# Performance work log

Hardware: AMD Instinct MI355X
Metric: run time of the kernel (lower is better)

Reference implementation:

```python
import jax, jax.numpy as jnp
import numpy as np

D_K = 64  # per-head dim, used as softmax scale (matches __init__ d_k)

def setup_inputs() -> dict:
    key = jax.random.key(0)
    kq, kk, kv, km = jax.random.split(key, 4)
    B, H, S, D = 2, 16, 2048, D_K
    q = jax.random.normal(kq, (B, H, S, D), dtype=jnp.float32)
    k = jax.random.normal(kk, (B, H, S, D), dtype=jnp.float32)
    v = jax.random.normal(kv, (B, H, S, D), dtype=jnp.float32)
    mask = jax.random.randint(km, (B, 1, S, S), 0, 2).astype(jnp.bool_)
    return {"q": q, "k": k, "v": v, "mask": mask}

def reference(q, k, v, mask):
    # attn = (q / sqrt(d_k)) @ k^T  -> [B,H,S,S]
    scale = 1.0 / jnp.sqrt(jnp.float32(D_K))
    attn = jnp.einsum("bhqd,bhkd->bhqk", q * scale, k)
    # faithful to torch masked_fill(mask, -1e-09) -- note tiny value, not -1e9
    attn = jnp.where(mask, jnp.float32(-1e-9), attn)
    weights = jax.nn.softmax(attn, axis=-1)  # dropout p=0.0 -> identity
    output = jnp.einsum("bhqk,bhkd->bhqd", weights, v)
    return (output, weights)
```

## Files before the change

### kernel.cpp

```cpp
#include <hip/hip_runtime.h>
#include <hip/hip_bf16.h>


namespace {

constexpr int kS = 2048;
constexpr int kD = 64;
constexpr int kBH = 32;
constexpr int kTQW = 16;
constexpr int kNW = 4;
constexpr int kTQB = kTQW * kNW;
constexpr int kChunk = 64;
constexpr int kNC = kS / kChunk;
constexpr int kNB = kBH * (kS / kTQB);
constexpr size_t kWOff = (size_t)kBH * kS * kD;

typedef __attribute__((ext_vector_type(8))) short bf16x8;
typedef __attribute__((ext_vector_type(4))) float f32x4;
typedef __attribute__((ext_vector_type(2))) unsigned u32x2;

__device__ inline short f2bf(float f) {
  union { float f; unsigned u; } x; x.f = f;
  return (short)((x.u + 0x7fffu + ((x.u >> 16) & 1u)) >> 16);
}

__device__ inline unsigned pk2bf(float a, float b) {
  return (unsigned)(unsigned short)f2bf(a) | ((unsigned)(unsigned short)f2bf(b) << 16);
}

__device__ inline bf16x8 cvt8(float4 a, float4 b, float scale) {
  bf16x8 f;
  f[0] = f2bf(a.x * scale); f[1] = f2bf(a.y * scale);
  f[2] = f2bf(a.z * scale); f[3] = f2bf(a.w * scale);
  f[4] = f2bf(b.x * scale); f[5] = f2bf(b.y * scale);
  f[6] = f2bf(b.z * scale); f[7] = f2bf(b.w * scale);
  return f;
}

__device__ inline void block_sync_lds() {
  asm volatile("s_waitcnt lgkmcnt(0)" ::: "memory");
  __builtin_amdgcn_s_barrier();
  asm volatile("" ::: "memory");
}

__global__ __launch_bounds__(256, 4) void attn_fused(
    const float* __restrict__ qg, const float* __restrict__ kg,
    const float* __restrict__ vg, const unsigned int* __restrict__ mg,
    float* __restrict__ outg) {
  __shared__ __align__(16) short SH[16384];
  short (*Kt0)[72] = (short(*)[72])SH;
  short (*Kt1)[72] = (short(*)[72])(SH + 4608);
  short (*Wts)[72] = (short(*)[72])(SH + 9216);
  unsigned char (*Msk0)[80] = (unsigned char(*)[80])(SH + 13824);
  unsigned char (*Msk1)[80] = (unsigned char(*)[80])(SH + 9216);

  const int tid  = threadIdx.x;
  const int wv   = tid >> 6;
  const int lane = tid & 63;
  const int l15  = lane & 15;
  const int quad = lane >> 4;

  const int bid  = blockIdx.x;
  const int work = ((bid & 7) << 7) | (bid >> 3);
  const int qt   = work & 31;
  const int bh   = work >> 5;
  const int b    = bh >> 4;
  const int q0b  = qt * kTQB;

  int allW32 = 1, allI32 = 1, allBF = 1;
#pragma unroll
  for (int i = 0; i < 64; ++i) {
    const unsigned u = mg[i];
    const unsigned lo = u & 0xFFFFu, hi = u >> 16;
    allW32 &= (int)(u == 0u || u == 0x3F800000u);
    allI32 &= (int)(u == 0u || u == 1u);
    allBF  &= (int)((lo == 0u || lo == 0x3F80u) && (hi == 0u || hi == 0x3F80u));
  }
  int msz;
  if (allI32)      msz = 4;
  else if (allW32) msz = 4;
  else if (allBF)  msz = 2;
  else             msz = 1;
  const unsigned char* mB = (const unsigned char*)mg + (size_t)b * kS * kS * msz;

  const float* qbase = qg + (size_t)bh * kS * kD;
  const float* kbase = kg + (size_t)bh * kS * kD;
  const float* vbase = vg + (size_t)bh * kS * kD;
  float* obase = outg + (size_t)bh * kS * kD;
  float* wbase = outg + kWOff + (size_t)bh * kS * kS;

  const int qrow = q0b + wv * kTQW + l15;
  const int mrow = wv * kTQW + l15;

  bf16x8 aq[2];
#pragma unroll
  for (int dh = 0; dh < 2; ++dh) {
    const float* p = qbase + (size_t)qrow * kD + dh * 32 + quad * 8;
    aq[dh] = cvt8(*(const float4*)p, *(const float4*)(p + 4), 0.125f);
  }

  const int si = tid >> 2;
  const int sj = (tid & 3) << 4;
  const int vd = (tid & 7) << 3;
  const int vk = (tid >> 3) << 1;
  float4 rk[4], rv[4];
  uint4 rmq;

  auto k_issue = [&](int c) {
    const float* p = kbase + (size_t)(c * kChunk + si) * kD + sj;
    rk[0] = *(const float4*)p;       rk[1] = *(const float4*)(p + 4);
    rk[2] = *(const float4*)(p + 8); rk[3] = *(const float4*)(p + 12);
  };
  auto k_write = [&](short (*Kdst)[72]) {
    *(bf16x8*)&Kdst[si][sj]     = cvt8(rk[0], rk[1], 1.0f);
    *(bf16x8*)&Kdst[si][sj + 8] = cvt8(rk[2], rk[3], 1.0f);
  };

  auto v_issue = [&](int c) {
    const float* p = vbase + (size_t)(c * kChunk + vk) * kD + vd;
    rv[0] = *(const float4*)p;        rv[1] = *(const float4*)(p + 4);
    rv[2] = *(const float4*)(p + kD); rv[3] = *(const float4*)(p + kD + 4);
  };
  auto v_write = [&]() {
    const float* lo = (const float*)&rv[0];
    const float* hi = (const float*)&rv[2];
#pragma unroll
    for (int d = 0; d < 8; ++d) {
      const int dd = vd + d;
      const int ps = (vk >> 1) ^ (((dd >> 3) & 7) << 2);
      const unsigned u = pk2bf(lo[d], hi[d]);
      *(unsigned*)&Kt1[dd][2 * ps] = u;
    }
  };

  auto m_issue = [&](int c) {
    if (msz == 1)
      rmq = *(const uint4*)(mB + (size_t)(q0b + si) * kS + (size_t)(c * kChunk + sj));
  };
  auto m_write = [&](unsigned char (*Mdst)[80], int c) {
    if (msz == 1) {
      *(uint4*)&Mdst[si][sj] = rmq;
    } else if (msz == 4) {
      const size_t eoff = (size_t)(q0b + si) * kS + (size_t)(c * kChunk + sj);
      const unsigned int* p = (const unsigned int*)mB + eoff;
      unsigned int* dst = (unsigned int*)&Mdst[si][sj];
#pragma unroll
      for (int g = 0; g < 4; ++g) {
        uint4 e = *(const uint4*)(p + 4 * g);
        dst[g] = (e.x ? 1u : 0u) | ((e.y ? 1u : 0u) << 8) |
                 ((e.z ? 1u : 0u) << 16) | ((e.w ? 1u : 0u) << 24);
      }
    } else {
      const size_t eoff = (size_t)(q0b + si) * kS + (size_t)(c * kChunk + sj);
      const unsigned int* p = (const unsigned int*)((const unsigned short*)mB + eoff);
      unsigned int* dst = (unsigned int*)&Mdst[si][sj];
#pragma unroll
      for (int g = 0; g < 4; ++g) {
        const unsigned int a = p[2 * g], cc = p[2 * g + 1];
        dst[g] = ((a & 0xFFFFu) ? 1u : 0u) | (((a >> 16) ? 1u : 0u) << 8) |
                 (((cc & 0xFFFFu) ? 1u : 0u) << 16) | (((cc >> 16) ? 1u : 0u) << 24);
      }
    }
  };

  float lsum = 0.f;
  k_issue(0); m_issue(0);
  k_write(Kt0); m_write(Msk0, 0);
  k_issue(1); m_issue(1);
  block_sync_lds();
  for (int c = 0; c < kNC; ++c) {
    short (*K)[72] = (c & 1) ? Kt1 : Kt0;
    const unsigned char (*M)[80] =
        (c & 1) ? (const unsigned char (*)[80])Msk1 : (const unsigned char (*)[80])Msk0;
    if (c + 1 < kNC) { k_write((c & 1) ? Kt0 : Kt1); m_write((c & 1) ? Msk0 : Msk1, c + 1); }
    if (c + 2 < kNC) { k_issue(c + 2); m_issue(c + 2); }
#pragma unroll
    for (int t = 0; t < 4; ++t) {
      bf16x8 f0 = *(const bf16x8*)&K[t * 16 + l15][quad * 8];
      bf16x8 f1 = *(const bf16x8*)&K[t * 16 + l15][32 + quad * 8];
      f32x4 acc = {0.f, 0.f, 0.f, 0.f};
      acc = __builtin_amdgcn_mfma_f32_16x16x32_bf16(f0, aq[0], acc, 0, 0, 0);
      acc = __builtin_amdgcn_mfma_f32_16x16x32_bf16(f1, aq[1], acc, 0, 0, 0);
      const unsigned mu = *(const unsigned*)&M[mrow][t * 16 + quad * 4];
#pragma unroll
      for (int r = 0; r < 4; ++r) {
        const float e = __expf(acc[r]);
        lsum += ((mu >> (8 * r)) & 0xFFu) ? 1.0f : e;
      }
    }
    block_sync_lds();
  }

  lsum += __shfl_xor(lsum, 16);
  lsum += __shfl_xor(lsum, 32);
  const float inv = 1.0f / lsum;

  f32x4 acco[4];
#pragma unroll
  for (int d = 0; d < 4; ++d) acco[d] = (f32x4){0.f, 0.f, 0.f, 0.f};

  k_issue(0); v_issue(0); m_issue(0);
  k_write(Kt0); v_write(); m_write(Msk0, 0);
  k_issue(1); v_issue(1); m_issue(1);
  block_sync_lds();
  float* const wrow = wbase + (size_t)qrow * kS;
  const int swz = (l15 & 7) << 3;
  for (int c = 0; c < kNC; ++c) {
#pragma unroll
    for (int t = 0; t < 4; ++t) {
      bf16x8 f0 = *(const bf16x8*)&Kt0[t * 16 + l15][quad * 8];
      bf16x8 f1 = *(const bf16x8*)&Kt0[t * 16 + l15][32 + quad * 8];
      f32x4 acc = {0.f, 0.f, 0.f, 0.f};
      acc = __builtin_amdgcn_mfma_f32_16x16x32_bf16(f0, aq[0], acc, 0, 0, 0);
      acc = __builtin_amdgcn_mfma_f32_16x16x32_bf16(f1, aq[1], acc, 0, 0, 0);
      const unsigned mu = *(const unsigned*)&Msk0[mrow][t * 16 + quad * 4];
      const float w0 = ((mu       & 0xFFu) ? 1.0f : __expf(acc[0])) * inv;
      const float w1 = ((mu >> 8  & 0xFFu) ? 1.0f : __expf(acc[1])) * inv;
      const float w2 = ((mu >> 16 & 0xFFu) ? 1.0f : __expf(acc[2])) * inv;
      const float w3 = ((mu >> 24        ) ? 1.0f : __expf(acc[3])) * inv;
      u32x2 uu = {pk2bf(w0, w1), pk2bf(w2, w3)};
      *(u32x2*)&Wts[wv * kTQW + l15][(t * 16 + quad * 4) ^ swz] = uu;
      f32x4 wq = {w0, w1, w2, w3};
      __builtin_nontemporal_store(wq, (f32x4*)(wrow + c * kChunk + t * 16 + quad * 4));
    }
    __builtin_amdgcn_s_setprio(1);
#pragma unroll
    for (int ks = 0; ks < 2; ++ks) {
      bf16x8 aw = *(const bf16x8*)&Wts[wv * kTQW + l15][(ks * 32 + quad * 8) ^ swz];
#pragma unroll
      for (int dt = 0; dt < 4; ++dt) {
        const int dd = dt * 16 + l15;
        const int psb = (ks * 16 + quad * 4) ^ (((dd >> 3) & 7) << 2);
        bf16x8 bv = *(const bf16x8*)&Kt1[dd][2 * psb];
        acco[dt] = __builtin_amdgcn_mfma_f32_16x16x32_bf16(bv, aw, acco[dt], 0, 0, 0);
      }
    }
    __builtin_amdgcn_s_setprio(0);
    block_sync_lds();
    if (c + 1 < kNC) { k_write(Kt0); v_write(); m_write(Msk0, c + 1); }
    if (c + 2 < kNC) { k_issue(c + 2); v_issue(c + 2); m_issue(c + 2); }
    block_sync_lds();
  }

#pragma unroll
  for (int dt = 0; dt < 4; ++dt) {
    f32x4 o = acco[dt];
    __builtin_nontemporal_store(o, (f32x4*)(obase + (size_t)qrow * kD + dt * 16 + quad * 4));
  }
}

}

extern "C" void kernel_launch(void* const* d_in, const int* in_sizes, int n_in,
                              void* d_out, int out_size, void* d_ws, size_t ws_size,
                              hipStream_t stream) {
  const float* q = (const float*)d_in[0];
  const float* k = (const float*)d_in[1];
  const float* v = (const float*)d_in[2];
  const unsigned int* mask = (const unsigned int*)d_in[3];
  float* out = (float*)d_out;
  attn_fused<<<dim3(kNB), dim3(256), 0, stream>>>(q, k, v, mask, out);
}
```

Measured before the change: 830.9 us.

## Double-buffer K/V in pass two, load mask into registers, feed PV MFMA from registers

The second pass now double-buffers both K and V in LDS with a single barrier per chunk, where it previously used one buffer and two barriers. The mask is read directly from global memory into per-lane registers instead of being staged through LDS. Probabilities are passed straight from the QK accumulator layout into 16x16x16 bf16 MFMAs for the PV product, which removes the weight round-trip through LDS. In exchange it issues twice as many smaller MFMAs, makes uncoalesced per-lane mask loads, and replaces the nontemporal weight stores with regular ones.

```diff
diff --git a/kernel.cpp b/kernel.cpp
--- a/kernel.cpp
+++ b/kernel.cpp
@@ -16,8 +16,8 @@
 constexpr size_t kWOff = (size_t)kBH * kS * kD;
 
 typedef __attribute__((ext_vector_type(8))) short bf16x8;
+typedef __attribute__((ext_vector_type(4))) short bf16x4;
 typedef __attribute__((ext_vector_type(4))) float f32x4;
-typedef __attribute__((ext_vector_type(2))) unsigned u32x2;
 
 __device__ inline short f2bf(float f) {
   union { float f; unsigned u; } x; x.f = f;
@@ -37,6 +37,22 @@
   return f;
 }
 
+__device__ inline f32x4 mfma32(bf16x8 a, bf16x8 b, f32x4 c) {
+  return __builtin_amdgcn_mfma_f32_16x16x32_bf16(a, b, c, 0, 0, 0);
+}
+
+__device__ inline f32x4 mfma16(bf16x4 a, bf16x4 b, f32x4 c) {
+#if __has_builtin(__builtin_amdgcn_mfma_f32_16x16x16bf16_1k)
+  return __builtin_amdgcn_mfma_f32_16x16x16bf16_1k(a, b, c, 0, 0, 0);
+#elif __has_builtin(__builtin_amdgcn_mfma_f32_16x16x16_bf16)
+  return __builtin_amdgcn_mfma_f32_16x16x16_bf16(a, b, c, 0, 0, 0);
+#else
+  f32x4 d = c;
+  asm volatile("v_mfma_f32_16x16x16_bf16 %0, %1, %2, %0" : "+v"(d) : "v"(a), "v"(b));
+  return d;
+#endif
+}
+
 __device__ inline void block_sync_lds() {
   asm volatile("s_waitcnt lgkmcnt(0)" ::: "memory");
   __builtin_amdgcn_s_barrier();
@@ -47,12 +63,11 @@
     const float* __restrict__ qg, const float* __restrict__ kg,
     const float* __restrict__ vg, const unsigned int* __restrict__ mg,
     float* __restrict__ outg) {
-  __shared__ __align__(16) short SH[16384];
-  short (*Kt0)[72] = (short(*)[72])SH;
-  short (*Kt1)[72] = (short(*)[72])(SH + 4608);
-  short (*Wts)[72] = (short(*)[72])(SH + 9216);
-  unsigned char (*Msk0)[80] = (unsigned char(*)[80])(SH + 13824);
-  unsigned char (*Msk1)[80] = (unsigned char(*)[80])(SH + 9216);
+  __shared__ __align__(16) short SH[18432];
+  short (*K0)[72] = (short(*)[72])(SH);
+  short (*K1)[72] = (short(*)[72])(SH + 4608);
+  short (*V0)[72] = (short(*)[72])(SH + 9216);
+  short (*V1)[72] = (short(*)[72])(SH + 13824);
 
   const int tid  = threadIdx.x;
   const int wv   = tid >> 6;
@@ -90,7 +105,6 @@
   float* wbase = outg + kWOff + (size_t)bh * kS * kS;
 
   const int qrow = q0b + wv * kTQW + l15;
-  const int mrow = wv * kTQW + l15;
 
   bf16x8 aq[2];
 #pragma unroll
@@ -104,7 +118,6 @@
   const int vd = (tid & 7) << 3;
   const int vk = (tid >> 3) << 1;
   float4 rk[4], rv[4];
-  uint4 rmq;
 
   auto k_issue = [&](int c) {
     const float* p = kbase + (size_t)(c * kChunk + si) * kD + sj;
@@ -121,71 +134,66 @@
     rv[0] = *(const float4*)p;        rv[1] = *(const float4*)(p + 4);
     rv[2] = *(const float4*)(p + kD); rv[3] = *(const float4*)(p + kD + 4);
   };
-  auto v_write = [&]() {
+  auto v_write = [&](short (*Vdst)[72]) {
     const float* lo = (const float*)&rv[0];
     const float* hi = (const float*)&rv[2];
 #pragma unroll
     for (int d = 0; d < 8; ++d) {
       const int dd = vd + d;
       const int ps = (vk >> 1) ^ (((dd >> 3) & 7) << 2);
-      const unsigned u = pk2bf(lo[d], hi[d]);
-      *(unsigned*)&Kt1[dd][2 * ps] = u;
-    }
-  };
-
+      *(unsigned*)&Vdst[dd][2 * ps] = pk2bf(lo[d], hi[d]);
+    }
+  };
+
+  uint4 mr[4];
+  unsigned mu[4];
   auto m_issue = [&](int c) {
-    if (msz == 1)
-      rmq = *(const uint4*)(mB + (size_t)(q0b + si) * kS + (size_t)(c * kChunk + sj));
-  };
-  auto m_write = [&](unsigned char (*Mdst)[80], int c) {
-    if (msz == 1) {
-      *(uint4*)&Mdst[si][sj] = rmq;
-    } else if (msz == 4) {
-      const size_t eoff = (size_t)(q0b + si) * kS + (size_t)(c * kChunk + sj);
-      const unsigned int* p = (const unsigned int*)mB + eoff;
-      unsigned int* dst = (unsigned int*)&Mdst[si][sj];
-#pragma unroll
-      for (int g = 0; g < 4; ++g) {
-        uint4 e = *(const uint4*)(p + 4 * g);
-        dst[g] = (e.x ? 1u : 0u) | ((e.y ? 1u : 0u) << 8) |
-                 ((e.z ? 1u : 0u) << 16) | ((e.w ? 1u : 0u) << 24);
-      }
-    } else {
-      const size_t eoff = (size_t)(q0b + si) * kS + (size_t)(c * kChunk + sj);
-      const unsigned int* p = (const unsigned int*)((const unsigned short*)mB + eoff);
-      unsigned int* dst = (unsigned int*)&Mdst[si][sj];
-#pragma unroll
-      for (int g = 0; g < 4; ++g) {
-        const unsigned int a = p[2 * g], cc = p[2 * g + 1];
-        dst[g] = ((a & 0xFFFFu) ? 1u : 0u) | (((a >> 16) ? 1u : 0u) << 8) |
-                 (((cc & 0xFFFFu) ? 1u : 0u) << 16) | (((cc >> 16) ? 1u : 0u) << 24);
+    const int col0 = c * kChunk + quad * 4;
+#pragma unroll
+    for (int t = 0; t < 4; ++t) {
+      const size_t e = (size_t)qrow * kS + col0 + t * 16;
+      if (msz == 1)      mr[t].x = *(const unsigned*)(mB + e);
+      else if (msz == 4) mr[t]   = *(const uint4*)((const unsigned*)mB + e);
+      else {
+        const unsigned* p = (const unsigned*)((const unsigned short*)mB + e);
+        mr[t].x = p[0]; mr[t].y = p[1];
+      }
+    }
+  };
+  auto m_conv = [&]() {
+#pragma unroll
+    for (int t = 0; t < 4; ++t) {
+      if (msz == 1)      mu[t] = mr[t].x;
+      else if (msz == 4) mu[t] = (mr[t].x ? 1u : 0u) | ((mr[t].y ? 1u : 0u) << 8) |
+                                 ((mr[t].z ? 1u : 0u) << 16) | ((mr[t].w ? 1u : 0u) << 24);
+      else {
+        const unsigned a = mr[t].x, bb = mr[t].y;
+        mu[t] = ((a & 0xFFFFu) ? 1u : 0u) | (((a >> 16) ? 1u : 0u) << 8) |
+                (((bb & 0xFFFFu) ? 1u : 0u) << 16) | (((bb >> 16) ? 1u : 0u) << 24);
       }
     }
   };
 
   float lsum = 0.f;
-  k_issue(0); m_issue(0);
-  k_write(Kt0); m_write(Msk0, 0);
-  k_issue(1); m_issue(1);
+  k_issue(0); k_write(K0); k_issue(1);
   block_sync_lds();
   for (int c = 0; c < kNC; ++c) {
-    short (*K)[72] = (c & 1) ? Kt1 : Kt0;
-    const unsigned char (*M)[80] =
-        (c & 1) ? (const unsigned char (*)[80])Msk1 : (const unsigned char (*)[80])Msk0;
-    if (c + 1 < kNC) { k_write((c & 1) ? Kt0 : Kt1); m_write((c & 1) ? Msk0 : Msk1, c + 1); }
-    if (c + 2 < kNC) { k_issue(c + 2); m_issue(c + 2); }
+    m_issue(c);
+    if (c + 1 < kNC) k_write((c & 1) ? K0 : K1);
+    if (c + 2 < kNC) k_issue(c + 2);
+    m_conv();
+    short (*K)[72] = (c & 1) ? K1 : K0;
 #pragma unroll
     for (int t = 0; t < 4; ++t) {
       bf16x8 f0 = *(const bf16x8*)&K[t * 16 + l15][quad * 8];
       bf16x8 f1 = *(const bf16x8*)&K[t * 16 + l15][32 + quad * 8];
       f32x4 acc = {0.f, 0.f, 0.f, 0.f};
-      acc = __builtin_amdgcn_mfma_f32_16x16x32_bf16(f0, aq[0], acc, 0, 0, 0);
-      acc = __builtin_amdgcn_mfma_f32_16x16x32_bf16(f1, aq[1], acc, 0, 0, 0);
-      const unsigned mu = *(const unsigned*)&M[mrow][t * 16 + quad * 4];
+      acc = mfma32(f0, aq[0], acc);
+      acc = mfma32(f1, aq[1], acc);
 #pragma unroll
       for (int r = 0; r < 4; ++r) {
         const float e = __expf(acc[r]);
-        lsum += ((mu >> (8 * r)) & 0xFFu) ? 1.0f : e;
+        lsum += ((mu[t] >> (8 * r)) & 0xFFu) ? 1.0f : e;
       }
     }
     block_sync_lds();
@@ -199,54 +207,48 @@
 #pragma unroll
   for (int d = 0; d < 4; ++d) acco[d] = (f32x4){0.f, 0.f, 0.f, 0.f};
 
-  k_issue(0); v_issue(0); m_issue(0);
-  k_write(Kt0); v_write(); m_write(Msk0, 0);
-  k_issue(1); v_issue(1); m_issue(1);
+  k_issue(0); v_issue(0);
+  k_write(K0); v_write(V0);
+  k_issue(1); v_issue(1);
   block_sync_lds();
   float* const wrow = wbase + (size_t)qrow * kS;
-  const int swz = (l15 & 7) << 3;
   for (int c = 0; c < kNC; ++c) {
-#pragma unroll
-    for (int t = 0; t < 4; ++t) {
-      bf16x8 f0 = *(const bf16x8*)&Kt0[t * 16 + l15][quad * 8];
-      bf16x8 f1 = *(const bf16x8*)&Kt0[t * 16 + l15][32 + quad * 8];
+    m_issue(c);
+    if (c + 1 < kNC) { k_write((c & 1) ? K0 : K1); v_write((c & 1) ? V0 : V1); }
+    if (c + 2 < kNC) { k_issue(c + 2); v_issue(c + 2); }
+    m_conv();
+    short (*K)[72] = (c & 1) ? K1 : K0;
+    short (*V)[72] = (c & 1) ? V1 : V0;
+    __builtin_amdgcn_s_setprio(1);
+#pragma unroll
+    for (int t = 0; t < 4; ++t) {
+      bf16x8 f0 = *(const bf16x8*)&K[t * 16 + l15][quad * 8];
+      bf16x8 f1 = *(const bf16x8*)&K[t * 16 + l15][32 + quad * 8];
       f32x4 acc = {0.f, 0.f, 0.f, 0.f};
-      acc = __builtin_amdgcn_mfma_f32_16x16x32_bf16(f0, aq[0], acc, 0, 0, 0);
-      acc = __builtin_amdgcn_mfma_f32_16x16x32_bf16(f1, aq[1], acc, 0, 0, 0);
-      const unsigned mu = *(const unsigned*)&Msk0[mrow][t * 16 + quad * 4];
-      const float w0 = ((mu       & 0xFFu) ? 1.0f : __expf(acc[0])) * inv;
-      const float w1 = ((mu >> 8  & 0xFFu) ? 1.0f : __expf(acc[1])) * inv;
-      const float w2 = ((mu >> 16 & 0xFFu) ? 1.0f : __expf(acc[2])) * inv;
-      const float w3 = ((mu >> 24        ) ? 1.0f : __expf(acc[3])) * inv;
-      u32x2 uu = {pk2bf(w0, w1), pk2bf(w2, w3)};
-      *(u32x2*)&Wts[wv * kTQW + l15][(t * 16 + quad * 4) ^ swz] = uu;
-      f32x4 wq = {w0, w1, w2, w3};
-      __builtin_nontemporal_store(wq, (f32x4*)(wrow + c * kChunk + t * 16 + quad * 4));
-    }
-    __builtin_amdgcn_s_setprio(1);
-#pragma unroll
-    for (int ks = 0; ks < 2; ++ks) {
-      bf16x8 aw = *(const bf16x8*)&Wts[wv * kTQW + l15][(ks * 32 + quad * 8) ^ swz];
+      acc = mfma32(f0, aq[0], acc);
+      acc = mfma32(f1, aq[1], acc);
+      const unsigned m = mu[t];
+      const float w0 = ((m       & 0xFFu) ? 1.0f : __expf(acc[0])) * inv;
+      const float w1 = ((m >> 8  & 0xFFu) ? 1.0f : __expf(acc[1])) * inv;
+      const float w2 = ((m >> 16 & 0xFFu) ? 1.0f : __expf(acc[2])) * inv;
+      const float w3 = ((m >> 24        ) ? 1.0f : __expf(acc[3])) * inv;
+      *(f32x4*)(wrow + c * kChunk + t * 16 + quad * 4) = (f32x4){w0, w1, w2, w3};
+      const bf16x4 wfrag = {f2bf(w0), f2bf(w1), f2bf(w2), f2bf(w3)};
 #pragma unroll
       for (int dt = 0; dt < 4; ++dt) {
         const int dd = dt * 16 + l15;
-        const int psb = (ks * 16 + quad * 4) ^ (((dd >> 3) & 7) << 2);
-        bf16x8 bv = *(const bf16x8*)&Kt1[dd][2 * psb];
-        acco[dt] = __builtin_amdgcn_mfma_f32_16x16x32_bf16(bv, aw, acco[dt], 0, 0, 0);
+        const int pp = (8 * t + 2 * quad) ^ (((dd >> 3) & 7) << 2);
+        const bf16x4 vfrag = *(const bf16x4*)&V[dd][2 * pp];
+        acco[dt] = mfma16(vfrag, wfrag, acco[dt]);
       }
     }
     __builtin_amdgcn_s_setprio(0);
     block_sync_lds();
-    if (c + 1 < kNC) { k_write(Kt0); v_write(); m_write(Msk0, c + 1); }
-    if (c + 2 < kNC) { k_issue(c + 2); v_issue(c + 2); m_issue(c + 2); }
-    block_sync_lds();
-  }
-
-#pragma unroll
-  for (int dt = 0; dt < 4; ++dt) {
-    f32x4 o = acco[dt];
-    __builtin_nontemporal_store(o, (f32x4*)(obase + (size_t)qrow * kD + dt * 16 + quad * 4));
-  }
+  }
+
+#pragma unroll
+  for (int dt = 0; dt < 4; ++dt)
+    *(f32x4*)(obase + (size_t)qrow * kD + dt * 16 + quad * 4) = acco[dt];
 }
 
 }
```

Measured after the change: 905.1 us. +8.9%, slower.
